# Kernel tuning notes

Measured on AMD Instinct MI355X. Metric: run time of the kernel, lower is better.

## Reference

```python
import jax, jax.numpy as jnp
import numpy as np


def setup_inputs() -> dict:
    key = jax.random.key(0)
    ks = jax.random.split(key, 8)
    B, S, Ta, D = 64, 512, 8, 768
    return {
        "memory": jax.random.normal(ks[0], (B, S, D), dtype=jnp.float32),
        "aspect_states": jax.random.normal(ks[1], (B, Ta, D), dtype=jnp.float32),
        "input_ids": jnp.ones((B, S), dtype=jnp.int64),
        "input_t_ids": jnp.ones((B, Ta), dtype=jnp.int64),
        "W1": jax.random.normal(ks[2], (3 * D, D), dtype=jnp.float32) * 0.02,
        "b1": jnp.zeros((D,), dtype=jnp.float32),
        "w2": jax.random.normal(ks[3], (D,), dtype=jnp.float32) * 0.02,
        "Wm": jax.random.normal(ks[4], (D, D), dtype=jnp.float32) * 0.02,
        "bm": jnp.zeros((D,), dtype=jnp.float32),
        "Wd": jax.random.normal(ks[5], (D, 3), dtype=jnp.float32) * 0.02,
        "bd": jnp.zeros((3,), dtype=jnp.float32),
    }


def reference(memory, aspect_states, input_ids, input_t_ids, W1, b1, w2, Wm, bm, Wd, bd):
    B, S, D = memory.shape
    memory_len = jnp.sum(input_ids != 0, axis=-1)          # [B]
    aspect_len = jnp.sum(input_t_ids != 0, axis=-1)        # [B]

    # v_a: mean-pooled aspect representation  [B, D]
    v_a = jnp.sum(aspect_states, axis=1) / aspect_len.astype(memory.dtype)[:, None]
    # v_s: mean-pooled sentence representation [B, D]
    v_s = jnp.sum(memory, axis=1) / memory_len.astype(memory.dtype)[:, None]

    # locationed_memory: memory[i, idx] *= 1 - idx/memory_len[i] for idx < memory_len[i]
    idx = jnp.arange(S, dtype=memory.dtype)                 # [S]
    mlen = memory_len.astype(memory.dtype)[:, None]         # [B, 1]
    loc = jnp.where(idx[None, :] < mlen, 1.0 - idx[None, :] / mlen, 1.0)  # [B, S]
    memory = memory * loc[:, :, None]

    # chunked linear1/linear2 scorer, vectorized:
    # c_t = w2 . tanh(W1 @ [m_t ; v_a ; v_s] + b1)
    W1_m, W1_a, W1_s = W1[:D], W1[D:2 * D], W1[2 * D:]
    ctx = v_a @ W1_a + v_s @ W1_s + b1                      # [B, D]
    h = jnp.tanh(jnp.einsum("bsd,de->bse", memory, W1_m) + ctx[:, None, :])
    scores = h @ w2                                         # [B, S]
    alpha = jax.nn.softmax(scores, axis=1)

    v_ts = jnp.einsum("bsd,bs->bd", memory, alpha)          # [B, D]
    v_ns = v_ts + v_s
    v_ms = jnp.tanh(v_ns @ Wm + bm)
    logits = v_ms @ Wd + bd                                 # [B, 3]
    return logits
```

## Files before the change

### kernel.cpp

```cpp
#include <hip/hip_runtime.h>
#include <hip/hip_bf16.h>


#define NB 64
#define NS 512
#define ND 768
#define NTA 8

typedef __attribute__((ext_vector_type(8))) __bf16 bf16x8;
typedef __attribute__((ext_vector_type(4))) float f32x4;

#define OFF_SCORES 0u
#define OFF_VS 131072u
#define OFF_VTS 327680u
#define OFF_CTX 524288u
#define OFF_U 720896u
#define ZERO_BYTES 917504u
#define OFF_VA 917504u
#define OFF_ALPHA 1114112u
#define OFF_LENS 1245184u
#define OFF_W1MT 1246208u
#define OFF_MP 2425856u

__device__ __forceinline__ float fast_tanh(float x) {
  x = fminf(fmaxf(x, -15.f), 15.f);
  float t = __expf(2.f * x);
  return __fdividef(t - 1.f, t + 1.f);
}

__device__ __forceinline__ unsigned bfpack2(float a, float b) {
  unsigned ua = __float_as_uint(a), ub = __float_as_uint(b);
  ua = (ua + 0x7FFFu + ((ua >> 16) & 1u)) >> 16;
  ub = (ub + 0x7FFFu + ((ub >> 16) & 1u)) >> 16;
  return ua | (ub << 16);
}

__device__ __forceinline__ unsigned short bf16b(float f) {
  unsigned u = __float_as_uint(f);
  u = (u + 0x7FFFu + ((u >> 16) & 1u)) >> 16;
  return (unsigned short)u;
}

__device__ __forceinline__ void async_copy16(const void* g, void* l) {
  __builtin_amdgcn_global_load_lds(
      (const __attribute__((address_space(1))) void*)g,
      (__attribute__((address_space(3))) void*)l, 16, 0, 0);
}

__global__ __launch_bounds__(128) void k_prep(const int* __restrict__ ids,
                                              const int* __restrict__ tids,
                                              const float* __restrict__ aspect,
                                              float* __restrict__ v_a,
                                              float* __restrict__ lens) {
  int b = blockIdx.x, tid = threadIdx.x;
  __shared__ int red[128];
  __shared__ float sh_inva;
  int cnt = 0;
  for (int j = tid; j < NS; j += 128) cnt += (ids[b * NS + j] != 0);
  red[tid] = cnt;
  __syncthreads();
  for (int s = 64; s > 0; s >>= 1) {
    if (tid < s) red[tid] += red[tid + s];
    __syncthreads();
  }
  if (tid == 0) {
    int mlen = red[0];
    int acnt = 0;
    for (int t = 0; t < NTA; ++t) acnt += (tids[b * NTA + t] != 0);
    lens[b] = (float)mlen;
    lens[64 + b] = 1.0f / (float)mlen;
    float inva = 1.0f / (float)acnt;
    lens[128 + b] = inva;
    sh_inva = inva;
  }
  __syncthreads();
  float inva = sh_inva;
  for (int j = tid; j < ND; j += 128) {
    float s = 0.f;
    for (int t = 0; t < NTA; ++t) s += aspect[((size_t)b * NTA + t) * ND + j];
    v_a[b * ND + j] = s * inva;
  }
}

__global__ __launch_bounds__(192) void k_vs_mprime(const float* __restrict__ memory,
                                                   const float* __restrict__ lens,
                                                   float* __restrict__ v_s,
                                                   unsigned short* __restrict__ mp) {
  int sc = blockIdx.x, b = blockIdx.y, tid = threadIdx.x;
  int d0 = tid * 4;
  float inv_mlen = lens[64 + b];
  float mlenf = lens[b];
  float s0 = 0, s1 = 0, s2 = 0, s3 = 0;
  for (int s = 0; s < 64; ++s) {
    int srow = sc * 64 + s;
    size_t row = (size_t)b * NS + srow;
    const float4 v = *(const float4*)(memory + row * ND + d0);
    s0 += v.x; s1 += v.y; s2 += v.z; s3 += v.w;
    float fs = (float)srow;
    float loc = (fs < mlenf) ? 1.0f - fs * inv_mlen : 1.0f;
    uint2 pk;
    pk.x = bfpack2(v.x * loc, v.y * loc);
    pk.y = bfpack2(v.z * loc, v.w * loc);
    *(uint2*)(mp + row * ND + d0) = pk;
  }
  float* p = v_s + b * ND + d0;
  atomicAdd(p + 0, s0 * inv_mlen);
  atomicAdd(p + 1, s1 * inv_mlen);
  atomicAdd(p + 2, s2 * inv_mlen);
  atomicAdd(p + 3, s3 * inv_mlen);
}

__global__ __launch_bounds__(256) void k_transpose(const float* __restrict__ W1,
                                                   unsigned short* __restrict__ w1mt) {
  __shared__ float tile[32][33];
  int bx = blockIdx.x, by = blockIdx.y;
  int tx = threadIdx.x, ty = threadIdx.y;
  for (int j = 0; j < 32; j += 8)
    tile[ty + j][tx] = W1[(size_t)(by * 32 + ty + j) * ND + bx * 32 + tx];
  __syncthreads();
  for (int j = 0; j < 32; j += 8)
    w1mt[(size_t)(bx * 32 + ty + j) * ND + by * 32 + tx] = bf16b(tile[tx][ty + j]);
}

__global__ __launch_bounds__(128) void k_ctx(const float* __restrict__ W1,
                                             const float* __restrict__ v_a,
                                             const float* __restrict__ v_s,
                                             float* __restrict__ ctx) {
  int et = blockIdx.x, b = blockIdx.y, dc = blockIdx.z, tid = threadIdx.x;
  __shared__ float vbuf[384];
  for (int j = tid; j < 384; j += 128) {
    int k = dc * 384 + j;
    vbuf[j] = (k < ND) ? v_a[b * ND + k] : v_s[b * ND + (k - ND)];
  }
  __syncthreads();
  int e = et * 128 + tid;
  float acc = 0.f;
  const float* Wk = W1 + (size_t)(ND + dc * 384) * ND + e;
#pragma unroll 8
  for (int j = 0; j < 384; ++j) acc += vbuf[j] * Wk[(size_t)j * ND];
  atomicAdd(&ctx[b * ND + e], acc);
}

__global__ __launch_bounds__(256) void k_gemm_scores(const unsigned short* __restrict__ mp,
                                                     const unsigned short* __restrict__ w1mt,
                                                     const float* __restrict__ ctx,
                                                     const float* __restrict__ b1,
                                                     const float* __restrict__ w2,
                                                     float* __restrict__ scores) {
  __shared__ char lds[32768];
  char* ldsA = lds;
  char* ldsB = lds + 16384;
  const int tid = threadIdx.x;
  const int wave = tid >> 6, lane = tid & 63;
  const int rt = blockIdx.x, et = blockIdx.y;
  const int row0 = rt * 128, n0 = et * 128;
  const int b = row0 >> 9;
  const int wm = wave & 1, wn = wave >> 1;

  const int lrow = lane >> 3;
  const int qlog = (lane & 7) ^ lrow;
  const char* Abase = (const char*)mp + (size_t)(row0 + lrow) * (ND * 2) + qlog * 16;
  const char* Bbase = (const char*)w1mt + (size_t)(n0 + lrow) * (ND * 2) + qlog * 16;

  f32x4 acc[4][4];
#pragma unroll
  for (int i = 0; i < 4; ++i)
#pragma unroll
    for (int t = 0; t < 4; ++t) acc[i][t] = (f32x4){0.f, 0.f, 0.f, 0.f};

  const int q2 = lane >> 4, c = lane & 15;
  int offA[4][2], offB[4][2];
#pragma unroll
  for (int i = 0; i < 4; ++i) {
    int ml = wm * 64 + i * 16 + c;
    offA[i][0] = ml * 128 + ((q2 ^ (ml & 7)) * 16);
    offA[i][1] = ml * 128 + (((4 + q2) ^ (ml & 7)) * 16);
    int nl = wn * 64 + i * 16 + c;
    offB[i][0] = nl * 128 + ((q2 ^ (nl & 7)) * 16);
    offB[i][1] = nl * 128 + (((4 + q2) ^ (nl & 7)) * 16);
  }

  for (int kb = 0; kb < ND * 2; kb += 128) {
#pragma unroll
    for (int i = 0; i < 4; ++i) {
      int g = wave * 4 + i;
      async_copy16(Abase + (size_t)g * 8 * (ND * 2) + kb, ldsA + g * 1024);
      async_copy16(Bbase + (size_t)g * 8 * (ND * 2) + kb, ldsB + g * 1024);
    }
    __syncthreads();
    bf16x8 af[2][4], bfr[2][4];
#pragma unroll
    for (int kk = 0; kk < 2; ++kk)
#pragma unroll
      for (int i = 0; i < 4; ++i) {
        af[kk][i] = *(const bf16x8*)(ldsA + offA[i][kk]);
        bfr[kk][i] = *(const bf16x8*)(ldsB + offB[i][kk]);
      }
#pragma unroll
    for (int kk = 0; kk < 2; ++kk)
#pragma unroll
      for (int i = 0; i < 4; ++i)
#pragma unroll
        for (int t = 0; t < 4; ++t)
          acc[i][t] = __builtin_amdgcn_mfma_f32_16x16x32_bf16(af[kk][i], bfr[kk][t], acc[i][t], 0, 0, 0);
    __syncthreads();
  }

  float ctxv[4], w2v[4];
#pragma unroll
  for (int t = 0; t < 4; ++t) {
    int n = n0 + wn * 64 + t * 16 + c;
    ctxv[t] = ctx[b * ND + n] + b1[n];
    w2v[t] = w2[n];
  }
#pragma unroll
  for (int i = 0; i < 4; ++i) {
#pragma unroll
    for (int r = 0; r < 4; ++r) {
      float s = 0.f;
#pragma unroll
      for (int t = 0; t < 4; ++t) s += fast_tanh(acc[i][t][r] + ctxv[t]) * w2v[t];
      s += __shfl_xor(s, 1, 64);
      s += __shfl_xor(s, 2, 64);
      s += __shfl_xor(s, 4, 64);
      s += __shfl_xor(s, 8, 64);
      if (c == 0) atomicAdd(&scores[row0 + wm * 64 + i * 16 + q2 * 4 + r], s);
    }
  }
}

__global__ __launch_bounds__(512) void k_softmax(const float* __restrict__ scores,
                                                 float* __restrict__ alpha) {
  int b = blockIdx.x, tid = threadIdx.x;
  int wid = tid >> 6, lane = tid & 63;
  __shared__ float red[8], red2[8];
  float v = scores[b * NS + tid];
  float m = v;
  for (int off = 1; off < 64; off <<= 1) m = fmaxf(m, __shfl_xor(m, off, 64));
  if (lane == 0) red[wid] = m;
  __syncthreads();
  if (tid == 0) {
    float mm = red[0];
    for (int i = 1; i < 8; ++i) mm = fmaxf(mm, red[i]);
    red[0] = mm;
  }
  __syncthreads();
  float M = red[0];
  float e = __expf(v - M);
  float s = e;
  for (int off = 1; off < 64; off <<= 1) s += __shfl_xor(s, off, 64);
  if (lane == 0) red2[wid] = s;
  __syncthreads();
  if (tid == 0) {
    float ss = 0.f;
    for (int i = 0; i < 8; ++i) ss += red2[i];
    red2[0] = ss;
  }
  __syncthreads();
  alpha[b * NS + tid] = e / red2[0];
}

__global__ __launch_bounds__(192) void k_vts(const unsigned short* __restrict__ mp,
                                             const float* __restrict__ alpha,
                                             float* __restrict__ v_ts) {
  int sc = blockIdx.x, b = blockIdx.y, tid = threadIdx.x;
  __shared__ float al[64];
  if (tid < 64) al[tid] = alpha[b * NS + sc * 64 + tid];
  __syncthreads();
  int d0 = tid * 4;
  float a0 = 0, a1 = 0, a2 = 0, a3 = 0;
  for (int s = 0; s < 64; ++s) {
    size_t row = (size_t)b * NS + sc * 64 + s;
    uint2 pk = *(const uint2*)(mp + row * ND + d0);
    float a = al[s];
    a0 += a * __uint_as_float(pk.x << 16);
    a1 += a * __uint_as_float(pk.x & 0xFFFF0000u);
    a2 += a * __uint_as_float(pk.y << 16);
    a3 += a * __uint_as_float(pk.y & 0xFFFF0000u);
  }
  float* p = v_ts + b * ND + d0;
  atomicAdd(p + 0, a0);
  atomicAdd(p + 1, a1);
  atomicAdd(p + 2, a2);
  atomicAdd(p + 3, a3);
}

__global__ __launch_bounds__(128) void k_final1(const float* __restrict__ v_ts,
                                                const float* __restrict__ v_s,
                                                const float* __restrict__ Wm,
                                                float* __restrict__ u) {
  int et = blockIdx.x, b = blockIdx.y, dc = blockIdx.z, tid = threadIdx.x;
  __shared__ float vbuf[192];
  for (int j = tid; j < 192; j += 128) {
    int d = dc * 192 + j;
    vbuf[j] = v_ts[b * ND + d] + v_s[b * ND + d];
  }
  __syncthreads();
  int e = et * 128 + tid;
  float acc = 0.f;
  const float* Wk = Wm + (size_t)(dc * 192) * ND + e;
#pragma unroll 8
  for (int j = 0; j < 192; ++j) acc += vbuf[j] * Wk[(size_t)j * ND];
  atomicAdd(&u[b * ND + e], acc);
}

__global__ __launch_bounds__(256) void k_final2(const float* __restrict__ u,
                                                const float* __restrict__ bm,
                                                const float* __restrict__ Wd,
                                                const float* __restrict__ bd,
                                                float* __restrict__ out) {
  int b = blockIdx.x, tid = threadIdx.x;
  int wid = tid >> 6, lane = tid & 63;
  __shared__ float red[4][3];
  float p0 = 0, p1 = 0, p2 = 0;
  for (int e = tid; e < ND; e += 256) {
    float vm = fast_tanh(u[b * ND + e] + bm[e]);
    p0 += vm * Wd[e * 3 + 0];
    p1 += vm * Wd[e * 3 + 1];
    p2 += vm * Wd[e * 3 + 2];
  }
  for (int off = 1; off < 64; off <<= 1) {
    p0 += __shfl_xor(p0, off, 64);
    p1 += __shfl_xor(p1, off, 64);
    p2 += __shfl_xor(p2, off, 64);
  }
  if (lane == 0) { red[wid][0] = p0; red[wid][1] = p1; red[wid][2] = p2; }
  __syncthreads();
  if (tid == 0) {
    out[b * 3 + 0] = red[0][0] + red[1][0] + red[2][0] + red[3][0] + bd[0];
    out[b * 3 + 1] = red[0][1] + red[1][1] + red[2][1] + red[3][1] + bd[1];
    out[b * 3 + 2] = red[0][2] + red[1][2] + red[2][2] + red[3][2] + bd[2];
  }
}

extern "C" void kernel_launch(void* const* d_in, const int* in_sizes, int n_in,
                              void* d_out, int out_size, void* d_ws, size_t ws_size,
                              hipStream_t stream) {
  const float* memory = (const float*)d_in[0];
  const float* aspect = (const float*)d_in[1];
  const int* ids = (const int*)d_in[2];
  const int* tids = (const int*)d_in[3];
  const float* W1 = (const float*)d_in[4];
  const float* b1 = (const float*)d_in[5];
  const float* w2 = (const float*)d_in[6];
  const float* Wm = (const float*)d_in[7];
  const float* bm = (const float*)d_in[8];
  const float* Wd = (const float*)d_in[9];
  const float* bd = (const float*)d_in[10];
  float* out = (float*)d_out;

  char* ws = (char*)d_ws;
  float* scores = (float*)(ws + OFF_SCORES);
  float* v_s = (float*)(ws + OFF_VS);
  float* v_ts = (float*)(ws + OFF_VTS);
  float* ctx = (float*)(ws + OFF_CTX);
  float* u = (float*)(ws + OFF_U);
  float* v_a = (float*)(ws + OFF_VA);
  float* alpha = (float*)(ws + OFF_ALPHA);
  float* lens = (float*)(ws + OFF_LENS);
  unsigned short* w1mt = (unsigned short*)(ws + OFF_W1MT);
  unsigned short* mp = (unsigned short*)(ws + OFF_MP);

  hipMemsetAsync(ws, 0, ZERO_BYTES, stream);

  k_prep<<<NB, 128, 0, stream>>>(ids, tids, aspect, v_a, lens);
  k_transpose<<<dim3(24, 24), dim3(32, 8), 0, stream>>>(W1, w1mt);
  k_vs_mprime<<<dim3(8, NB), 192, 0, stream>>>(memory, lens, v_s, mp);
  k_ctx<<<dim3(6, NB, 4), 128, 0, stream>>>(W1, v_a, v_s, ctx);
  k_gemm_scores<<<dim3(256, 6), 256, 0, stream>>>(mp, w1mt, ctx, b1, w2, scores);
  k_softmax<<<NB, 512, 0, stream>>>(scores, alpha);
  k_vts<<<dim3(8, NB), 192, 0, stream>>>(mp, alpha, v_ts);
  k_final1<<<dim3(6, NB, 4), 128, 0, stream>>>(v_ts, v_s, Wm, u);
  k_final2<<<NB, 256, 0, stream>>>(u, bm, Wd, bd, out);
}
```

Baseline: 323.4 us.

## Fuse prep kernels, fold softmax into vts, enlarge GEMM row tile

Merges the W1 transpose and length/aspect prep into a single launch, and folds the softmax into the weighted-sum kernel so each block recomputes the max and sum itself. The GEMM tile grows to 256 rows with a rasterized grid order and 2-block occupancy. The s-chunk in k_vs_mprime and k_vts_sm is halved to give more blocks. These cut launch count and alpha round-trips and raise B-tile reuse, at the cost of redundant softmax reductions and more registers and LDS in the GEMM.

```diff
diff --git a/kernel.cpp b/kernel.cpp
--- a/kernel.cpp
+++ b/kernel.cpp
@@ -17,7 +17,6 @@
 #define OFF_U 720896u
 #define ZERO_BYTES 917504u
 #define OFF_VA 917504u
-#define OFF_ALPHA 1114112u
 #define OFF_LENS 1245184u
 #define OFF_W1MT 1246208u
 #define OFF_MP 2425856u
@@ -47,38 +46,52 @@
       (__attribute__((address_space(3))) void*)l, 16, 0, 0);
 }
 
-__global__ __launch_bounds__(128) void k_prep(const int* __restrict__ ids,
-                                              const int* __restrict__ tids,
-                                              const float* __restrict__ aspect,
-                                              float* __restrict__ v_a,
-                                              float* __restrict__ lens) {
-  int b = blockIdx.x, tid = threadIdx.x;
-  __shared__ int red[128];
-  __shared__ float sh_inva;
-  int cnt = 0;
-  for (int j = tid; j < NS; j += 128) cnt += (ids[b * NS + j] != 0);
-  red[tid] = cnt;
-  __syncthreads();
-  for (int s = 64; s > 0; s >>= 1) {
-    if (tid < s) red[tid] += red[tid + s];
-    __syncthreads();
-  }
-  if (tid == 0) {
-    int mlen = red[0];
-    int acnt = 0;
-    for (int t = 0; t < NTA; ++t) acnt += (tids[b * NTA + t] != 0);
-    lens[b] = (float)mlen;
-    lens[64 + b] = 1.0f / (float)mlen;
-    float inva = 1.0f / (float)acnt;
-    lens[128 + b] = inva;
-    sh_inva = inva;
-  }
-  __syncthreads();
-  float inva = sh_inva;
-  for (int j = tid; j < ND; j += 128) {
-    float s = 0.f;
-    for (int t = 0; t < NTA; ++t) s += aspect[((size_t)b * NTA + t) * ND + j];
-    v_a[b * ND + j] = s * inva;
+__global__ __launch_bounds__(256) void k_pre(const float* __restrict__ W1,
+                                             unsigned short* __restrict__ w1mt,
+                                             const int* __restrict__ ids,
+                                             const int* __restrict__ tids,
+                                             const float* __restrict__ aspect,
+                                             float* __restrict__ v_a,
+                                             float* __restrict__ lens) {
+  int bid = blockIdx.x, tid = threadIdx.x;
+  if (bid < 576) {
+    __shared__ float tile[32][33];
+    int bx = bid % 24, by = bid / 24;
+    int tx = tid & 31, ty = tid >> 5;
+    for (int j = 0; j < 32; j += 8)
+      tile[ty + j][tx] = W1[(size_t)(by * 32 + ty + j) * ND + bx * 32 + tx];
+    __syncthreads();
+    for (int j = 0; j < 32; j += 8)
+      w1mt[(size_t)(bx * 32 + ty + j) * ND + by * 32 + tx] = bf16b(tile[tx][ty + j]);
+  } else {
+    int b = bid - 576;
+    __shared__ int red[256];
+    __shared__ float sh_inva;
+    int cnt = 0;
+    for (int j = tid; j < NS; j += 256) cnt += (ids[b * NS + j] != 0);
+    red[tid] = cnt;
+    __syncthreads();
+    for (int s = 128; s > 0; s >>= 1) {
+      if (tid < s) red[tid] += red[tid + s];
+      __syncthreads();
+    }
+    if (tid == 0) {
+      int mlen = red[0];
+      int acnt = 0;
+      for (int t = 0; t < NTA; ++t) acnt += (tids[b * NTA + t] != 0);
+      lens[b] = (float)mlen;
+      lens[64 + b] = 1.0f / (float)mlen;
+      float inva = 1.0f / (float)acnt;
+      lens[128 + b] = inva;
+      sh_inva = inva;
+    }
+    __syncthreads();
+    float inva = sh_inva;
+    for (int j = tid; j < ND; j += 256) {
+      float s = 0.f;
+      for (int t = 0; t < NTA; ++t) s += aspect[((size_t)b * NTA + t) * ND + j];
+      v_a[b * ND + j] = s * inva;
+    }
   }
 }
 
@@ -91,8 +104,8 @@
   float inv_mlen = lens[64 + b];
   float mlenf = lens[b];
   float s0 = 0, s1 = 0, s2 = 0, s3 = 0;
-  for (int s = 0; s < 64; ++s) {
-    int srow = sc * 64 + s;
+  for (int s = 0; s < 32; ++s) {
+    int srow = sc * 32 + s;
     size_t row = (size_t)b * NS + srow;
     const float4 v = *(const float4*)(memory + row * ND + d0);
     s0 += v.x; s1 += v.y; s2 += v.z; s3 += v.w;
@@ -110,18 +123,6 @@
   atomicAdd(p + 3, s3 * inv_mlen);
 }
 
-__global__ __launch_bounds__(256) void k_transpose(const float* __restrict__ W1,
-                                                   unsigned short* __restrict__ w1mt) {
-  __shared__ float tile[32][33];
-  int bx = blockIdx.x, by = blockIdx.y;
-  int tx = threadIdx.x, ty = threadIdx.y;
-  for (int j = 0; j < 32; j += 8)
-    tile[ty + j][tx] = W1[(size_t)(by * 32 + ty + j) * ND + bx * 32 + tx];
-  __syncthreads();
-  for (int j = 0; j < 32; j += 8)
-    w1mt[(size_t)(bx * 32 + ty + j) * ND + by * 32 + tx] = bf16b(tile[tx][ty + j]);
-}
-
 __global__ __launch_bounds__(128) void k_ctx(const float* __restrict__ W1,
                                              const float* __restrict__ v_a,
                                              const float* __restrict__ v_s,
@@ -141,19 +142,19 @@
   atomicAdd(&ctx[b * ND + e], acc);
 }
 
-__global__ __launch_bounds__(256) void k_gemm_scores(const unsigned short* __restrict__ mp,
-                                                     const unsigned short* __restrict__ w1mt,
-                                                     const float* __restrict__ ctx,
-                                                     const float* __restrict__ b1,
-                                                     const float* __restrict__ w2,
-                                                     float* __restrict__ scores) {
-  __shared__ char lds[32768];
+__global__ __launch_bounds__(256, 2) void k_gemm_scores(const unsigned short* __restrict__ mp,
+                                                        const unsigned short* __restrict__ w1mt,
+                                                        const float* __restrict__ ctx,
+                                                        const float* __restrict__ b1,
+                                                        const float* __restrict__ w2,
+                                                        float* __restrict__ scores) {
+  __shared__ char lds[49152];
   char* ldsA = lds;
-  char* ldsB = lds + 16384;
+  char* ldsB = lds + 32768;
   const int tid = threadIdx.x;
   const int wave = tid >> 6, lane = tid & 63;
-  const int rt = blockIdx.x, et = blockIdx.y;
-  const int row0 = rt * 128, n0 = et * 128;
+  const int et = blockIdx.x, rt = blockIdx.y;
+  const int row0 = rt * 256, n0 = et * 128;
   const int b = row0 >> 9;
   const int wm = wave & 1, wn = wave >> 1;
 
@@ -162,47 +163,51 @@
   const char* Abase = (const char*)mp + (size_t)(row0 + lrow) * (ND * 2) + qlog * 16;
   const char* Bbase = (const char*)w1mt + (size_t)(n0 + lrow) * (ND * 2) + qlog * 16;
 
-  f32x4 acc[4][4];
-#pragma unroll
-  for (int i = 0; i < 4; ++i)
+  f32x4 acc[8][4];
+#pragma unroll
+  for (int i = 0; i < 8; ++i)
 #pragma unroll
     for (int t = 0; t < 4; ++t) acc[i][t] = (f32x4){0.f, 0.f, 0.f, 0.f};
 
   const int q2 = lane >> 4, c = lane & 15;
-  int offA[4][2], offB[4][2];
-#pragma unroll
-  for (int i = 0; i < 4; ++i) {
-    int ml = wm * 64 + i * 16 + c;
-    offA[i][0] = ml * 128 + ((q2 ^ (ml & 7)) * 16);
-    offA[i][1] = ml * 128 + (((4 + q2) ^ (ml & 7)) * 16);
-    int nl = wn * 64 + i * 16 + c;
-    offB[i][0] = nl * 128 + ((q2 ^ (nl & 7)) * 16);
-    offB[i][1] = nl * 128 + (((4 + q2) ^ (nl & 7)) * 16);
+  int offA0[8], offB0[4];
+#pragma unroll
+  for (int i = 0; i < 8; ++i) {
+    int ml = wm * 128 + i * 16 + c;
+    offA0[i] = ml * 128 + ((q2 ^ (ml & 7)) * 16);
+  }
+#pragma unroll
+  for (int t = 0; t < 4; ++t) {
+    int nl = wn * 64 + t * 16 + c;
+    offB0[t] = nl * 128 + ((q2 ^ (nl & 7)) * 16);
   }
 
   for (int kb = 0; kb < ND * 2; kb += 128) {
+#pragma unroll
+    for (int i = 0; i < 8; ++i) {
+      int g = wave * 8 + i;
+      async_copy16(Abase + (size_t)g * 8 * (ND * 2) + kb, ldsA + g * 1024);
+    }
 #pragma unroll
     for (int i = 0; i < 4; ++i) {
       int g = wave * 4 + i;
-      async_copy16(Abase + (size_t)g * 8 * (ND * 2) + kb, ldsA + g * 1024);
       async_copy16(Bbase + (size_t)g * 8 * (ND * 2) + kb, ldsB + g * 1024);
     }
     __syncthreads();
-    bf16x8 af[2][4], bfr[2][4];
-#pragma unroll
-    for (int kk = 0; kk < 2; ++kk)
-#pragma unroll
-      for (int i = 0; i < 4; ++i) {
-        af[kk][i] = *(const bf16x8*)(ldsA + offA[i][kk]);
-        bfr[kk][i] = *(const bf16x8*)(ldsB + offB[i][kk]);
+#pragma unroll
+    for (int kk = 0; kk < 2; ++kk) {
+      const int x = kk * 64;
+      bf16x8 bfrag[4];
+#pragma unroll
+      for (int t = 0; t < 4; ++t) bfrag[t] = *(const bf16x8*)(ldsB + (offB0[t] ^ x));
+#pragma unroll
+      for (int i = 0; i < 8; ++i) {
+        bf16x8 afrag = *(const bf16x8*)(ldsA + (offA0[i] ^ x));
+#pragma unroll
+        for (int t = 0; t < 4; ++t)
+          acc[i][t] = __builtin_amdgcn_mfma_f32_16x16x32_bf16(afrag, bfrag[t], acc[i][t], 0, 0, 0);
       }
-#pragma unroll
-    for (int kk = 0; kk < 2; ++kk)
-#pragma unroll
-      for (int i = 0; i < 4; ++i)
-#pragma unroll
-        for (int t = 0; t < 4; ++t)
-          acc[i][t] = __builtin_amdgcn_mfma_f32_16x16x32_bf16(af[kk][i], bfr[kk][t], acc[i][t], 0, 0, 0);
+    }
     __syncthreads();
   }
 
@@ -214,7 +219,7 @@
     w2v[t] = w2[n];
   }
 #pragma unroll
-  for (int i = 0; i < 4; ++i) {
+  for (int i = 0; i < 8; ++i) {
 #pragma unroll
     for (int r = 0; r < 4; ++r) {
       float s = 0.f;
@@ -224,53 +229,44 @@
       s += __shfl_xor(s, 2, 64);
       s += __shfl_xor(s, 4, 64);
       s += __shfl_xor(s, 8, 64);
-      if (c == 0) atomicAdd(&scores[row0 + wm * 64 + i * 16 + q2 * 4 + r], s);
-    }
-  }
-}
-
-__global__ __launch_bounds__(512) void k_softmax(const float* __restrict__ scores,
-                                                 float* __restrict__ alpha) {
-  int b = blockIdx.x, tid = threadIdx.x;
+      if (c == 0) atomicAdd(&scores[row0 + wm * 128 + i * 16 + q2 * 4 + r], s);
+    }
+  }
+}
+
+__global__ __launch_bounds__(192) void k_vts_sm(const unsigned short* __restrict__ mp,
+                                                const float* __restrict__ scores,
+                                                float* __restrict__ v_ts) {
+  int sc = blockIdx.x, b = blockIdx.y, tid = threadIdx.x;
   int wid = tid >> 6, lane = tid & 63;
-  __shared__ float red[8], red2[8];
-  float v = scores[b * NS + tid];
-  float m = v;
+  __shared__ float sm[3], ss[3];
+  __shared__ float al[32];
+  float v[3];
+#pragma unroll
+  for (int k = 0; k < 3; ++k) {
+    int j = tid + k * 192;
+    v[k] = (j < NS) ? scores[b * NS + j] : -1e30f;
+  }
+  float m = fmaxf(fmaxf(v[0], v[1]), v[2]);
   for (int off = 1; off < 64; off <<= 1) m = fmaxf(m, __shfl_xor(m, off, 64));
-  if (lane == 0) red[wid] = m;
-  __syncthreads();
-  if (tid == 0) {
-    float mm = red[0];
-    for (int i = 1; i < 8; ++i) mm = fmaxf(mm, red[i]);
-    red[0] = mm;
-  }
-  __syncthreads();
-  float M = red[0];
-  float e = __expf(v - M);
-  float s = e;
-  for (int off = 1; off < 64; off <<= 1) s += __shfl_xor(s, off, 64);
-  if (lane == 0) red2[wid] = s;
-  __syncthreads();
-  if (tid == 0) {
-    float ss = 0.f;
-    for (int i = 0; i < 8; ++i) ss += red2[i];
-    red2[0] = ss;
-  }
-  __syncthreads();
-  alpha[b * NS + tid] = e / red2[0];
-}
-
-__global__ __launch_bounds__(192) void k_vts(const unsigned short* __restrict__ mp,
-                                             const float* __restrict__ alpha,
-                                             float* __restrict__ v_ts) {
-  int sc = blockIdx.x, b = blockIdx.y, tid = threadIdx.x;
-  __shared__ float al[64];
-  if (tid < 64) al[tid] = alpha[b * NS + sc * 64 + tid];
-  __syncthreads();
+  if (lane == 0) sm[wid] = m;
+  __syncthreads();
+  float M = fmaxf(fmaxf(sm[0], sm[1]), sm[2]);
+  float e = 0.f;
+#pragma unroll
+  for (int k = 0; k < 3; ++k)
+    if (tid + k * 192 < NS) e += __expf(v[k] - M);
+  for (int off = 1; off < 64; off <<= 1) e += __shfl_xor(e, off, 64);
+  if (lane == 0) ss[wid] = e;
+  __syncthreads();
+  float invS = 1.0f / (ss[0] + ss[1] + ss[2]);
+  if (tid < 32) al[tid] = __expf(scores[b * NS + sc * 32 + tid] - M) * invS;
+  __syncthreads();
+
   int d0 = tid * 4;
   float a0 = 0, a1 = 0, a2 = 0, a3 = 0;
-  for (int s = 0; s < 64; ++s) {
-    size_t row = (size_t)b * NS + sc * 64 + s;
+  for (int s = 0; s < 32; ++s) {
+    size_t row = (size_t)b * NS + sc * 32 + s;
     uint2 pk = *(const uint2*)(mp + row * ND + d0);
     float a = al[s];
     a0 += a * __uint_as_float(pk.x << 16);
@@ -356,20 +352,17 @@
   float* ctx = (float*)(ws + OFF_CTX);
   float* u = (float*)(ws + OFF_U);
   float* v_a = (float*)(ws + OFF_VA);
-  float* alpha = (float*)(ws + OFF_ALPHA);
   float* lens = (float*)(ws + OFF_LENS);
   unsigned short* w1mt = (unsigned short*)(ws + OFF_W1MT);
   unsigned short* mp = (unsigned short*)(ws + OFF_MP);
 
   hipMemsetAsync(ws, 0, ZERO_BYTES, stream);
 
-  k_prep<<<NB, 128, 0, stream>>>(ids, tids, aspect, v_a, lens);
-  k_transpose<<<dim3(24, 24), dim3(32, 8), 0, stream>>>(W1, w1mt);
-  k_vs_mprime<<<dim3(8, NB), 192, 0, stream>>>(memory, lens, v_s, mp);
+  k_pre<<<640, 256, 0, stream>>>(W1, w1mt, ids, tids, aspect, v_a, lens);
+  k_vs_mprime<<<dim3(16, NB), 192, 0, stream>>>(memory, lens, v_s, mp);
   k_ctx<<<dim3(6, NB, 4), 128, 0, stream>>>(W1, v_a, v_s, ctx);
-  k_gemm_scores<<<dim3(256, 6), 256, 0, stream>>>(mp, w1mt, ctx, b1, w2, scores);
-  k_softmax<<<NB, 512, 0, stream>>>(scores, alpha);
-  k_vts<<<dim3(8, NB), 192, 0, stream>>>(mp, alpha, v_ts);
+  k_gemm_scores<<<dim3(6, 128), 256, 0, stream>>>(mp, w1mt, ctx, b1, w2, scores);
+  k_vts_sm<<<dim3(16, NB), 192, 0, stream>>>(mp, scores, v_ts);
   k_final1<<<dim3(6, NB, 4), 128, 0, stream>>>(v_ts, v_s, Wm, u);
   k_final2<<<NB, 256, 0, stream>>>(u, bm, Wd, bd, out);
 }
```

Measured after the change: 325.9 us. Within noise of the previous version (+0.8%).
